# Kernel tuning notes

Hardware: AMD Instinct MI355X
Metric: run time of the kernel (lower is better)

Reference implementation:

```python
import jax, jax.numpy as jnp
import numpy as np

S, H = 8192, 2048

def setup_inputs() -> dict:
    key = jax.random.key(0)
    k1, k2, k3 = jax.random.split(key, 3)
    hidden = jax.random.normal(k1, (1, H), dtype=jnp.float32)
    encoder_outputs = jax.random.normal(k2, (S, 1, H), dtype=jnp.float32)
    W = jax.random.normal(k3, (H, H), dtype=jnp.float32) * (1.0 / np.sqrt(H))
    b = jnp.zeros((H,), dtype=jnp.float32)
    return {"hidden": hidden, "encoder_outputs": encoder_outputs, "W": W, "b": b}

def reference(hidden, encoder_outputs, W, b):
    # hidden: [1, H] -> [H]; encoder_outputs: [S, 1, H] -> [S, H]
    h = hidden[0]                      # [H]
    enc = encoder_outputs[:, 0, :]     # [S, H]
    # method='general': energy_i = h . (W @ enc_i + b)
    proj = jnp.einsum('sh,kh->sk', enc, W) + b   # [S, H] (Linear: x @ W.T + b)
    energies = proj @ h                          # [S]
    attn = jax.nn.softmax(energies, axis=0)      # softmax over seq dim
    return attn[None, None, :]                   # [1, 1, S]
```

## Files before the change

kernel.cpp:

```cpp
#include <hip/hip_runtime.h>


#define Hdim 2048
#define Sdim 8192
#define NBLK2 2048

__global__ void kv_matvec(const float* __restrict__ W, const float* __restrict__ hid,
                          float* __restrict__ v) {
    int b = blockIdx.x;
    int c0 = (b & 7) * 256 + (b >> 3) * 8;
    int t = threadIdx.x;
    int cp = (t & 1) * 4;
    int rl = t >> 1;
    float4 acc = {0.f, 0.f, 0.f, 0.f};
#pragma unroll
    for (int i = 0; i < 8; ++i) {
        int k = rl + 256 * i;
        float hk = hid[k];
        float4 w = *reinterpret_cast<const float4*>(W + (size_t)k * Hdim + c0 + cp);
        acc.x += w.x * hk;
        acc.y += w.y * hk;
        acc.z += w.z * hk;
        acc.w += w.w * hk;
    }
    __shared__ float4 red[512];
    red[t] = acc;
    __syncthreads();
    for (int s = 128; s > 0; s >>= 1) {
        if (rl < s) {
            float4 o = red[t + 2 * s];
            float4 m = red[t];
            m.x += o.x; m.y += o.y; m.z += o.z; m.w += o.w;
            red[t] = m;
        }
        __syncthreads();
    }
    if (t < 2) *reinterpret_cast<float4*>(v + c0 + t * 4) = red[t];
}

__global__ void k2_energies(const float* __restrict__ enc, const float* __restrict__ v,
                            float* __restrict__ e, float2* __restrict__ pairs) {
    int t = threadIdx.x;
    int lane = t & 63;
    int wave = t >> 6;
    int s = blockIdx.x * 4 + wave;
    const float* row = enc + (size_t)s * Hdim;
    float acc = 0.f;
#pragma unroll
    for (int i = 0; i < 8; ++i) {
        int idx = i * 256 + lane * 4;
        float4 a = *reinterpret_cast<const float4*>(row + idx);
        float4 w = *reinterpret_cast<const float4*>(v + idx);
        acc += a.x * w.x + a.y * w.y + a.z * w.z + a.w * w.w;
    }
#pragma unroll
    for (int off = 32; off > 0; off >>= 1) acc += __shfl_xor(acc, off, 64);
    __shared__ float se[4];
    if (lane == 0) {
        e[s] = acc;
        se[wave] = acc;
    }
    __syncthreads();
    if (t == 0) {
        float m = fmaxf(fmaxf(se[0], se[1]), fmaxf(se[2], se[3]));
        float l = __expf(se[0] - m) + __expf(se[1] - m) + __expf(se[2] - m) + __expf(se[3] - m);
        pairs[blockIdx.x] = make_float2(m, l);
    }
}

__global__ void k3_norm(const float* __restrict__ e, const float2* __restrict__ pairs,
                        float* __restrict__ out) {
    int t = threadIdx.x;
    int lane = t & 63, wave = t >> 6;
    float m = -1e30f;
    float2 p[8];
#pragma unroll
    for (int j = 0; j < 8; ++j) {
        p[j] = pairs[t + 256 * j];
        m = fmaxf(m, p[j].x);
    }
#pragma unroll
    for (int off = 32; off > 0; off >>= 1) m = fmaxf(m, __shfl_xor(m, off, 64));
    __shared__ float red[4];
    __shared__ float bcastM, bcastL;
    if (lane == 0) red[wave] = m;
    __syncthreads();
    if (t == 0) bcastM = fmaxf(fmaxf(red[0], red[1]), fmaxf(red[2], red[3]));
    __syncthreads();
    float M = bcastM;
    float l = 0.f;
#pragma unroll
    for (int j = 0; j < 8; ++j) l += p[j].y * __expf(p[j].x - M);
#pragma unroll
    for (int off = 32; off > 0; off >>= 1) l += __shfl_xor(l, off, 64);
    __syncthreads();
    if (lane == 0) red[wave] = l;
    __syncthreads();
    if (t == 0) bcastL = red[0] + red[1] + red[2] + red[3];
    __syncthreads();
    float invL = 1.0f / bcastL;
    int idx = blockIdx.x * 256 + t;
    out[idx] = __expf(e[idx] - M) * invL;
}

extern "C" void kernel_launch(void* const* d_in, const int* in_sizes, int n_in,
                              void* d_out, int out_size, void* d_ws, size_t ws_size,
                              hipStream_t stream) {
    const float* hid = (const float*)d_in[0];
    const float* enc = (const float*)d_in[1];
    const float* W   = (const float*)d_in[2];
    float* out = (float*)d_out;
    float* ws = (float*)d_ws;

    float* v = ws;
    float* e = v + Hdim;
    float2* pairs = (float2*)(e + Sdim);

    kv_matvec<<<256, 512, 0, stream>>>(W, hid, v);
    k2_energies<<<NBLK2, 256, 0, stream>>>(enc, v, e, pairs);
    k3_norm<<<32, 256, 0, stream>>>(e, pairs, out);
}
```

Before: 25.81 us.

## Fuse matvec and energy kernels with flag-based inter-block sync and prefetch

```diff
diff --git a/kernel.cpp b/kernel.cpp
--- a/kernel.cpp
+++ b/kernel.cpp
@@ -3,104 +3,143 @@
 
 #define Hdim 2048
 #define Sdim 8192
-#define NBLK2 2048
+#define MAGIC 0x7E57C0DE
 
-__global__ void kv_matvec(const float* __restrict__ W, const float* __restrict__ hid,
-                          float* __restrict__ v) {
-    int b = blockIdx.x;
-    int c0 = (b & 7) * 256 + (b >> 3) * 8;
-    int t = threadIdx.x;
-    int cp = (t & 1) * 4;
-    int rl = t >> 1;
-    float4 acc = {0.f, 0.f, 0.f, 0.f};
+__global__ __launch_bounds__(256, 4) void k_fused(
+    const float* __restrict__ W, const float* __restrict__ hid,
+    const float* __restrict__ enc, float* __restrict__ v,
+    float* __restrict__ e, float2* __restrict__ pairs, int* __restrict__ flags) {
+    __shared__ float v_lds[Hdim];
+    __shared__ float se[8];
+    int t = threadIdx.x, b = blockIdx.x;
+    int lane = t & 63, wv = t >> 6;
+
+    if (b < 256) {
+        int c0 = ((b & 7) << 8) + ((b >> 3) << 3);
+        int cp = (t & 1) * 4;
+        int rl = t >> 1;
+        float4 acc = {0.f, 0.f, 0.f, 0.f};
+#pragma unroll
+        for (int i = 0; i < 16; ++i) {
+            int k = rl + (i << 7);
+            float hk = hid[k];
+            float4 w = *reinterpret_cast<const float4*>(W + (size_t)k * Hdim + c0 + cp);
+            acc.x += w.x * hk; acc.y += w.y * hk; acc.z += w.z * hk; acc.w += w.w * hk;
+        }
+        float4* red = reinterpret_cast<float4*>(v_lds);
+        red[t] = acc;
+        __syncthreads();
+        for (int s2 = 64; s2 > 0; s2 >>= 1) {
+            if (rl < s2) {
+                float4 o = red[t + 2 * s2]; float4 m = red[t];
+                m.x += o.x; m.y += o.y; m.z += o.z; m.w += o.w;
+                red[t] = m;
+            }
+            __syncthreads();
+        }
+        if (t < 2) {
+            float4 r = red[t];
+            __hip_atomic_store(&v[c0 + cp + 0], r.x, __ATOMIC_RELAXED, __HIP_MEMORY_SCOPE_AGENT);
+            __hip_atomic_store(&v[c0 + cp + 1], r.y, __ATOMIC_RELAXED, __HIP_MEMORY_SCOPE_AGENT);
+            __hip_atomic_store(&v[c0 + cp + 2], r.z, __ATOMIC_RELAXED, __HIP_MEMORY_SCOPE_AGENT);
+            __hip_atomic_store(&v[c0 + cp + 3], r.w, __ATOMIC_RELAXED, __HIP_MEMORY_SCOPE_AGENT);
+        }
+        asm volatile("s_waitcnt vmcnt(0)" ::: "memory");
+        if (t == 0)
+            __hip_atomic_store(&flags[b], MAGIC, __ATOMIC_RELAXED, __HIP_MEMORY_SCOPE_AGENT);
+        __syncthreads();
+    }
+
+    size_t s0 = (size_t)b * 8 + wv * 2;
+    const float* r0 = enc + s0 * Hdim;
+    float4 pf[8];
+#pragma unroll
+    for (int i = 0; i < 8; ++i)
+        pf[i] = *reinterpret_cast<const float4*>(r0 + i * 256 + lane * 4);
+
+    {
+        int f;
+        do {
+            f = __hip_atomic_load(&flags[t], __ATOMIC_RELAXED, __HIP_MEMORY_SCOPE_AGENT);
+            if (f != MAGIC) __builtin_amdgcn_s_sleep(8);
+        } while (f != MAGIC);
+    }
+    __syncthreads();
+    asm volatile("" ::: "memory");
+
+#pragma unroll
+    for (int j = 0; j < 8; ++j) {
+        int idx = j * 256 + t;
+        v_lds[idx] = __hip_atomic_load(&v[idx], __ATOMIC_RELAXED, __HIP_MEMORY_SCOPE_AGENT);
+    }
+    __syncthreads();
+
+    float acc0 = 0.f;
 #pragma unroll
     for (int i = 0; i < 8; ++i) {
-        int k = rl + 256 * i;
-        float hk = hid[k];
-        float4 w = *reinterpret_cast<const float4*>(W + (size_t)k * Hdim + c0 + cp);
-        acc.x += w.x * hk;
-        acc.y += w.y * hk;
-        acc.z += w.z * hk;
-        acc.w += w.w * hk;
+        float4 a = pf[i];
+        float4 w = *reinterpret_cast<float4*>(&v_lds[i * 256 + lane * 4]);
+        acc0 += a.x * w.x + a.y * w.y + a.z * w.z + a.w * w.w;
     }
-    __shared__ float4 red[512];
-    red[t] = acc;
-    __syncthreads();
-    for (int s = 128; s > 0; s >>= 1) {
-        if (rl < s) {
-            float4 o = red[t + 2 * s];
-            float4 m = red[t];
-            m.x += o.x; m.y += o.y; m.z += o.z; m.w += o.w;
-            red[t] = m;
-        }
-        __syncthreads();
-    }
-    if (t < 2) *reinterpret_cast<float4*>(v + c0 + t * 4) = red[t];
-}
+#pragma unroll
+    for (int off = 32; off > 0; off >>= 1) acc0 += __shfl_xor(acc0, off, 64);
+    if (lane == 0) { e[s0] = acc0; se[wv * 2] = acc0; }
 
-__global__ void k2_energies(const float* __restrict__ enc, const float* __restrict__ v,
-                            float* __restrict__ e, float2* __restrict__ pairs) {
-    int t = threadIdx.x;
-    int lane = t & 63;
-    int wave = t >> 6;
-    int s = blockIdx.x * 4 + wave;
-    const float* row = enc + (size_t)s * Hdim;
-    float acc = 0.f;
+    const float* r1 = r0 + Hdim;
+    float acc1 = 0.f;
 #pragma unroll
     for (int i = 0; i < 8; ++i) {
-        int idx = i * 256 + lane * 4;
-        float4 a = *reinterpret_cast<const float4*>(row + idx);
-        float4 w = *reinterpret_cast<const float4*>(v + idx);
-        acc += a.x * w.x + a.y * w.y + a.z * w.z + a.w * w.w;
+        float4 a = *reinterpret_cast<const float4*>(r1 + i * 256 + lane * 4);
+        float4 w = *reinterpret_cast<float4*>(&v_lds[i * 256 + lane * 4]);
+        acc1 += a.x * w.x + a.y * w.y + a.z * w.z + a.w * w.w;
     }
 #pragma unroll
-    for (int off = 32; off > 0; off >>= 1) acc += __shfl_xor(acc, off, 64);
-    __shared__ float se[4];
-    if (lane == 0) {
-        e[s] = acc;
-        se[wave] = acc;
-    }
+    for (int off = 32; off > 0; off >>= 1) acc1 += __shfl_xor(acc1, off, 64);
+    if (lane == 0) { e[s0 + 1] = acc1; se[wv * 2 + 1] = acc1; }
     __syncthreads();
+
     if (t == 0) {
-        float m = fmaxf(fmaxf(se[0], se[1]), fmaxf(se[2], se[3]));
-        float l = __expf(se[0] - m) + __expf(se[1] - m) + __expf(se[2] - m) + __expf(se[3] - m);
-        pairs[blockIdx.x] = make_float2(m, l);
+        float m = se[0];
+#pragma unroll
+        for (int j = 1; j < 8; ++j) m = fmaxf(m, se[j]);
+        float l = 0.f;
+#pragma unroll
+        for (int j = 0; j < 8; ++j) l += __expf(se[j] - m);
+        pairs[b] = make_float2(m, l);
     }
 }
 
 __global__ void k3_norm(const float* __restrict__ e, const float2* __restrict__ pairs,
-                        float* __restrict__ out) {
-    int t = threadIdx.x;
-    int lane = t & 63, wave = t >> 6;
+                        float* __restrict__ out, int* __restrict__ flags) {
+    int t = threadIdx.x, lane = t & 63, wv = t >> 6;
+    __shared__ float red[4];
+    __shared__ float bM, bL;
+    float2 p[4];
     float m = -1e30f;
-    float2 p[8];
 #pragma unroll
-    for (int j = 0; j < 8; ++j) {
-        p[j] = pairs[t + 256 * j];
-        m = fmaxf(m, p[j].x);
-    }
+    for (int j = 0; j < 4; ++j) { p[j] = pairs[j * 256 + t]; m = fmaxf(m, p[j].x); }
 #pragma unroll
     for (int off = 32; off > 0; off >>= 1) m = fmaxf(m, __shfl_xor(m, off, 64));
-    __shared__ float red[4];
-    __shared__ float bcastM, bcastL;
-    if (lane == 0) red[wave] = m;
+    if (lane == 0) red[wv] = m;
     __syncthreads();
-    if (t == 0) bcastM = fmaxf(fmaxf(red[0], red[1]), fmaxf(red[2], red[3]));
+    if (t == 0) bM = fmaxf(fmaxf(red[0], red[1]), fmaxf(red[2], red[3]));
     __syncthreads();
-    float M = bcastM;
+    float M = bM;
     float l = 0.f;
 #pragma unroll
-    for (int j = 0; j < 8; ++j) l += p[j].y * __expf(p[j].x - M);
+    for (int j = 0; j < 4; ++j) l += p[j].y * __expf(p[j].x - M);
 #pragma unroll
     for (int off = 32; off > 0; off >>= 1) l += __shfl_xor(l, off, 64);
     __syncthreads();
-    if (lane == 0) red[wave] = l;
+    if (lane == 0) red[wv] = l;
     __syncthreads();
-    if (t == 0) bcastL = red[0] + red[1] + red[2] + red[3];
+    if (t == 0) bL = red[0] + red[1] + red[2] + red[3];
     __syncthreads();
-    float invL = 1.0f / bcastL;
+    float invL = 1.0f / bL;
     int idx = blockIdx.x * 256 + t;
     out[idx] = __expf(e[idx] - M) * invL;
+    if (blockIdx.x == 0)
+        __hip_atomic_store(&flags[t], 0, __ATOMIC_RELAXED, __HIP_MEMORY_SCOPE_AGENT);
 }
 
 extern "C" void kernel_launch(void* const* d_in, const int* in_sizes, int n_in,
@@ -115,8 +154,8 @@
     float* v = ws;
     float* e = v + Hdim;
     float2* pairs = (float2*)(e + Sdim);
+    int* flags = (int*)(pairs + 1024);
 
-    kv_matvec<<<256, 512, 0, stream>>>(W, hid, v);
-    k2_energies<<<NBLK2, 256, 0, stream>>>(enc, v, e, pairs);
-    k3_norm<<<32, 256, 0, stream>>>(e, pairs, out);
+    k_fused<<<1024, 256, 0, stream>>>(W, hid, enc, v, e, pairs, flags);
+    k3_norm<<<32, 256, 0, stream>>>(e, pairs, out, flags);
 }
```

New measurement: 31.11 us. +20.5%, slower.
